# Kernel optimization log

Measured on AMD Instinct MI355X. Metric: run time of the kernel, lower is better.

## Reference

```python
import jax, jax.numpy as jnp
import numpy as np

LMAX = 5
RESOLUTION = 12
ASPECT_RATIO = 2
BATCH = 256
NB = 2 * RESOLUTION                       # res_beta = 24
NA = round(2 * ASPECT_RATIO * RESOLUTION)  # res_alpha = res_gamma = 48
DIM = sum((2 * l + 1) ** 2 for l in range(LMAX + 1))  # 286

# normalize2mom constant for tanh: (E_{z~N(0,1)}[tanh(z)^2])^{-1/2}
_x = np.linspace(-12.0, 12.0, 1_000_001)
_pdf = np.exp(-0.5 * _x * _x) / np.sqrt(2.0 * np.pi)
ACT_CST = float(np.trapz(np.tanh(_x) ** 2 * _pdf, _x) ** -0.5)  # ~1.5927


def _su2_generators(j):
    m = np.arange(-j, j)
    raising = np.diag(-np.sqrt(j * (j + 1) - m * (m + 1)), k=-1).astype(complex)
    m = np.arange(-j + 1, j + 1)
    lowering = np.diag(np.sqrt(j * (j + 1) - m * (m - 1)), k=1).astype(complex)
    m = np.arange(-j, j + 1)
    return np.stack([0.5 * (raising + lowering), np.diag(1j * m), -0.5j * (raising - lowering)])


def _q_real_to_complex(l):
    q = np.zeros((2 * l + 1, 2 * l + 1), dtype=complex)
    for m in range(-l, 0):
        q[l + m, l + abs(m)] = 1 / np.sqrt(2)
        q[l + m, l - abs(m)] = -1j / np.sqrt(2)
    q[l, l] = 1
    for m in range(1, l + 1):
        q[l + m, l + abs(m)] = (-1) ** m / np.sqrt(2)
        q[l + m, l - abs(m)] = 1j * (-1) ** m / np.sqrt(2)
    return (-1j) ** l * q


def _so3_generators(l):
    X = _su2_generators(l)
    Q = _q_real_to_complex(l)
    return np.real(np.conj(Q.T)[None] @ X @ Q[None])  # real [3, 2l+1, 2l+1]


def _expm_angles(A, t):
    """exp(t_n * A) for real antisymmetric A via eigendecomposition. -> [n, d, d] real"""
    vals, vecs = np.linalg.eig(A.astype(complex))
    inv = np.linalg.inv(vecs)
    phases = np.exp(t[:, None] * vals[None, :])  # [n, d]
    return np.real(np.einsum('ij,nj,jk->nik', vecs, phases, inv))


def _build_D_and_qw():
    # Euler angle grids (e3nn SO3Grid convention)
    b = (np.arange(NB) + 0.5) / NB * np.pi          # beta   [nb]
    a = np.arange(NA) / NA * 2.0 * np.pi            # alpha=gamma [na]
    blocks = []
    for l in range(LMAX + 1):
        X = _so3_generators(l)
        Ra = _expm_angles(X[1], a)   # exp(alpha * X1)  [na,d,d]
        Rb = _expm_angles(X[0], b)   # exp(beta  * X0)  [nb,d,d]
        # D^l(a,b,c) = Ra[a] @ Rb[b] @ Ra[c]
        Dl = np.einsum('xij,yjk,zkl->xyzil', Ra, Rb, Ra)
        blocks.append(np.sqrt(2 * l + 1) * Dl.reshape(NA, NB, NA, -1))
    D = np.concatenate(blocks, axis=-1).astype(np.float32)  # [na, nb, na, dim]
    # lie_learn / Kostelec-Rockmore quadrature weights for beta
    bb = NB // 2
    k = np.arange(bb)
    j = np.arange(2 * bb)
    w = (2.0 / bb) * np.sin(np.pi * (2 * j + 1) / (4.0 * bb)) * np.sum(
        (1.0 / (2 * k + 1))[None, :]
        * np.sin((2 * j[:, None] + 1) * (2 * k[None, :] + 1) * np.pi / (4.0 * bb)),
        axis=1,
    )
    w = w / (2.0 * (2 * bb) ** 2)
    qw = (w * NB ** 2 / NA ** 2).astype(np.float32)  # [nb]
    return jnp.asarray(D), jnp.asarray(qw)


def setup_inputs() -> dict:
    key = jax.random.key(0)
    features = jax.random.normal(key, (BATCH, DIM), dtype=jnp.float32)
    D, qw = _build_D_and_qw()
    return {"features": features, "D": D, "qw": qw}


def reference(features, D, qw):
    dim = D.shape[-1]
    s = jnp.sqrt(jnp.asarray(dim, features.dtype))
    # to_grid: [B, dim] x [na, nb, na, dim] -> [B, na, nb, na]
    g = jnp.einsum('bi,xyzi->bxyz', features, D) / s
    # normalized pointwise nonlinearity on SO(3) samples
    g = ACT_CST * jnp.tanh(g)
    # from_grid: quadrature-weighted projection back onto flat Wigner basis
    return jnp.einsum('bxyz,y,xyzi->bi', g, qw, D) * s
```

## Files before the change

### kernel.cpp

```cpp
#include <hip/hip_runtime.h>
#include <hip/hip_bf16.h>

#define DIM    286
#define DIMP   288
#define NZTOT  55296
#define NBATCH 256
#define NB_    24
#define NA_    48
#define ZC     32
#define NTILES 1728
#define NCHUNK 192
#define TILES_PER_WG 9
#define S_CONST 16.911534525287763f
#define INV_S   0.05913123959890826f
#define ACT_CST 1.5927f

typedef short bf16x8 __attribute__((ext_vector_type(8)));
typedef float f32x4  __attribute__((ext_vector_type(4)));

#define WS_FBF  0u
#define WS_DBF  147456u
#define WS_DT   (WS_DBF + 31850496u)
#define WS_PART (WS_DT + 31850496u)

typedef const __attribute__((address_space(1))) char GA;
typedef __attribute__((address_space(3))) char LA;
__device__ __forceinline__ void gload_lds16(const void* g, void* l) {
    __builtin_amdgcn_global_load_lds((GA*)g, (LA*)l, 16, 0, 0);
}

__global__ void k_prep(const float* __restrict__ F, const float* __restrict__ D,
                       const float* __restrict__ qw,
                       __hip_bfloat16* __restrict__ Fbf,
                       __hip_bfloat16* __restrict__ Dbf, __hip_bfloat16* __restrict__ Dt2) {
    __shared__ float T[32][305];
    __shared__ float qs[24];
    int t = threadIdx.x;
    int bid = blockIdx.x;
    if (bid >= NTILES) {
        int o = (bid - NTILES) * 256 + t;
        int row = o / DIMP, col = o % DIMP;
        float v = (col < DIM) ? F[row * DIM + col] * INV_S : 0.f;
        Fbf[o] = __float2bfloat16(v);
        return;
    }
    int z0 = bid * 32;
    if (t < 24) qs[t] = qw[t] * S_CONST;
    const float4* Df = (const float4*)(D + (size_t)z0 * DIM);
    for (int k = 0; k < 9; ++k) {
        int idx = t + k * 256;
        if (idx < 2288) {
            float4 v = Df[idx];
            int e = idx * 4;
            int z = e / DIM, i = e % DIM;
            __hip_bfloat162 lo, hi;
            lo.x = __float2bfloat16(v.x); lo.y = __float2bfloat16(v.y);
            hi.x = __float2bfloat16(v.z); hi.y = __float2bfloat16(v.w);
            T[z][i] = v.x; T[z][i + 1] = v.y;
            *(__hip_bfloat162*)(Dbf + (size_t)(z0 + z) * DIMP + i) = lo;
            if (i == 284) {
                T[z + 1][0] = v.z; T[z + 1][1] = v.w;
                *(__hip_bfloat162*)(Dbf + (size_t)(z0 + z + 1) * DIMP) = hi;
            } else {
                T[z][i + 2] = v.z; T[z][i + 3] = v.w;
                *(__hip_bfloat162*)(Dbf + (size_t)(z0 + z) * DIMP + i + 2) = hi;
            }
        }
    }
    if (t < 32) {
        __hip_bfloat162 zz; zz.x = __float2bfloat16(0.f); zz.y = zz.x;
        *(__hip_bfloat162*)(Dbf + (size_t)(z0 + t) * DIMP + DIM) = zz;
    }
    __syncthreads();
    for (int s = 0; s < 5; ++s) {
        int idx = t + s * 256;
        if (idx < 1152) {
            int i = idx >> 2, zc = idx & 3;
            __hip_bfloat16 o8[8];
            #pragma unroll
            for (int j = 0; j < 8; ++j) {
                int zl = zc * 8 + j;
                int y = ((z0 + zl) / NA_) % NB_;
                o8[j] = __float2bfloat16(T[zl][i] * qs[y]);
            }
            *(bf16x8*)(Dt2 + ((size_t)bid * DIMP + i) * ZC + zc * 8) = *(const bf16x8*)o8;
        }
    }
}

__launch_bounds__(256, 4)
__global__ void k_main(const __hip_bfloat16* __restrict__ Fbf,
                       const __hip_bfloat16* __restrict__ Dbf,
                       const __hip_bfloat16* __restrict__ Dt2,
                       __hip_bfloat16* __restrict__ part) {
    __shared__ __align__(16) __hip_bfloat16 Ds[32][288];
    __shared__ __align__(16) __hip_bfloat16 Dts[288][32];
    __shared__ __align__(16) __hip_bfloat16 Gs[4][16][32];

    int t = threadIdx.x;
    int wave = t >> 6, lane = t & 63, ln = lane & 15, q = lane >> 4;

    bf16x8 fa[9];
    int row = blockIdx.y * 64 + wave * 16 + ln;
    const __hip_bfloat16* fp = Fbf + (size_t)row * DIMP + q * 8;
    #pragma unroll
    for (int ks = 0; ks < 9; ++ks) fa[ks] = *(const bf16x8*)(fp + ks * 32);

    f32x4 acc[18];
    #pragma unroll
    for (int n = 0; n < 18; ++n) acc[n] = (f32x4){0.f, 0.f, 0.f, 0.f};

    #pragma unroll 1
    for (int k = 0; k < TILES_PER_WG; ++k) {
        int tz = blockIdx.x + k * NCHUNK;
        {
            const char* src; char* dst;
            if (wave < 2) {
                src = (const char*)(Dbf + (size_t)tz * ZC * DIMP) + wave * 9216 + lane * 16;
                dst = ((char*)&Ds[0][0]) + wave * 9216;
            } else {
                src = (const char*)(Dt2 + (size_t)tz * DIMP * ZC) + (wave - 2) * 9216 + lane * 16;
                dst = ((char*)&Dts[0][0]) + (wave - 2) * 9216;
            }
            #pragma unroll
            for (int j = 0; j < 9; ++j)
                gload_lds16(src + j * 1024, dst + j * 1024);
        }
        asm volatile("s_waitcnt vmcnt(0)" ::: "memory");
        __syncthreads();
        f32x4 g0 = (f32x4){0.f,0.f,0.f,0.f}, g1 = (f32x4){0.f,0.f,0.f,0.f};
        #pragma unroll
        for (int ks = 0; ks < 9; ++ks) {
            bf16x8 b0 = *(const bf16x8*)(&Ds[ln][ks * 32 + q * 8]);
            bf16x8 b1 = *(const bf16x8*)(&Ds[16 + ln][ks * 32 + q * 8]);
            g0 = __builtin_amdgcn_mfma_f32_16x16x32_bf16(fa[ks], b0, g0, 0, 0, 0);
            g1 = __builtin_amdgcn_mfma_f32_16x16x32_bf16(fa[ks], b1, g1, 0, 0, 0);
        }
        #pragma unroll
        for (int nf = 0; nf < 2; ++nf) {
            #pragma unroll
            for (int r = 0; r < 4; ++r) {
                float x = (nf == 0) ? g0[r] : g1[r];
                float a = fabsf(x);
                float e = __expf(-2.f * a);
                float th = (1.f - e) / (1.f + e);
                float v = copysignf(ACT_CST * th, x);
                Gs[wave][q * 4 + r][nf * 16 + ln] = __float2bfloat16(v);
            }
        }
        bf16x8 a2 = *(const bf16x8*)(&Gs[wave][ln][q * 8]);
        #pragma unroll
        for (int nf = 0; nf < 18; ++nf) {
            bf16x8 b2 = *(const bf16x8*)(&Dts[nf * 16 + ln][q * 8]);
            acc[nf] = __builtin_amdgcn_mfma_f32_16x16x32_bf16(a2, b2, acc[nf], 0, 0, 0);
        }
        __syncthreads();
    }
    __hip_bfloat16* pb = part + ((size_t)blockIdx.x * NBATCH + blockIdx.y * 64 + wave * 16) * DIMP;
    #pragma unroll
    for (int nf = 0; nf < 18; ++nf) {
        #pragma unroll
        for (int r = 0; r < 4; ++r) {
            pb[(size_t)(q * 4 + r) * DIMP + nf * 16 + ln] = __float2bfloat16(acc[nf][r]);
        }
    }
}

__global__ void k_reduce(const __hip_bfloat16* __restrict__ part, float* __restrict__ out) {
    __shared__ float red[3][16][8];
    int t = threadIdx.x, wave = t >> 6, lane = t & 63;
    int j = lane & 15;
    int zg = wave * 4 + (lane >> 4);
    int o8 = blockIdx.x * 16 + j;
    int b = o8 / 36, c8 = o8 % 36;
    const __hip_bfloat16* p = part + (size_t)b * DIMP + c8 * 8;
    float s[8];
    #pragma unroll
    for (int kk = 0; kk < 8; ++kk) s[kk] = 0.f;
    #pragma unroll 4
    for (int ii = 0; ii < 12; ++ii) {
        bf16x8 v = *(const bf16x8*)(p + (size_t)(zg * 12 + ii) * NBATCH * DIMP);
        #pragma unroll
        for (int kk = 0; kk < 8; ++kk) {
            __hip_bfloat16 h; *(short*)&h = v[kk];
            s[kk] += __bfloat162float(h);
        }
    }
    #pragma unroll
    for (int kk = 0; kk < 8; ++kk) {
        s[kk] += __shfl_down(s[kk], 16);
        s[kk] += __shfl_down(s[kk], 32);
    }
    if (wave > 0 && lane < 16) {
        #pragma unroll
        for (int kk = 0; kk < 8; ++kk) red[wave - 1][lane][kk] = s[kk];
    }
    __syncthreads();
    if (wave == 0 && lane < 16) {
        #pragma unroll
        for (int w = 0; w < 3; ++w)
            #pragma unroll
            for (int kk = 0; kk < 8; ++kk) s[kk] += red[w][lane][kk];
        int i0 = c8 * 8;
        #pragma unroll
        for (int kk = 0; kk < 8; ++kk)
            if (i0 + kk < DIM) out[b * DIM + i0 + kk] = s[kk];
    }
}

extern "C" void kernel_launch(void* const* d_in, const int* in_sizes, int n_in,
                              void* d_out, int out_size, void* d_ws, size_t ws_size,
                              hipStream_t stream) {
    const float* F  = (const float*)d_in[0];
    const float* D  = (const float*)d_in[1];
    const float* qw = (const float*)d_in[2];
    char* ws = (char*)d_ws;
    __hip_bfloat16* Fbf = (__hip_bfloat16*)(ws + WS_FBF);
    __hip_bfloat16* Dbf = (__hip_bfloat16*)(ws + WS_DBF);
    __hip_bfloat16* Dt2 = (__hip_bfloat16*)(ws + WS_DT);
    __hip_bfloat16* part = (__hip_bfloat16*)(ws + WS_PART);

    k_prep<<<NTILES + 288, 256, 0, stream>>>(F, D, qw, Fbf, Dbf, Dt2);
    k_main<<<dim3(NCHUNK, 4), 256, 0, stream>>>(Fbf, Dbf, Dt2, part);
    k_reduce<<<576, 256, 0, stream>>>(part, (float*)d_out);
}
```

Before: 159.3 us.

## Process 32 batch rows per wave to halve D tile reloads

Each wave now handles two 16-row batch fragments instead of one, so each workgroup covers 128 batch rows and the grid's y dimension drops from 4 to 2. Each D/Dt tile loaded into LDS is reused across twice as many MFMAs, which halves global/L2 traffic for the large D arrays. The cost is doubled accumulator registers (36 f32x4 plus 18 A fragments), lower occupancy (launch bounds 2), and half as many workgroups, which reduces latency hiding.

```diff
diff --git a/kernel.cpp b/kernel.cpp
--- a/kernel.cpp
+++ b/kernel.cpp
@@ -88,27 +88,32 @@
     }
 }
 
-__launch_bounds__(256, 4)
+__launch_bounds__(256, 2)
 __global__ void k_main(const __hip_bfloat16* __restrict__ Fbf,
                        const __hip_bfloat16* __restrict__ Dbf,
                        const __hip_bfloat16* __restrict__ Dt2,
                        __hip_bfloat16* __restrict__ part) {
     __shared__ __align__(16) __hip_bfloat16 Ds[32][288];
     __shared__ __align__(16) __hip_bfloat16 Dts[288][32];
-    __shared__ __align__(16) __hip_bfloat16 Gs[4][16][32];
+    __shared__ __align__(16) __hip_bfloat16 Gs[4][32][32];
 
     int t = threadIdx.x;
     int wave = t >> 6, lane = t & 63, ln = lane & 15, q = lane >> 4;
 
-    bf16x8 fa[9];
-    int row = blockIdx.y * 64 + wave * 16 + ln;
-    const __hip_bfloat16* fp = Fbf + (size_t)row * DIMP + q * 8;
-    #pragma unroll
-    for (int ks = 0; ks < 9; ++ks) fa[ks] = *(const bf16x8*)(fp + ks * 32);
-
-    f32x4 acc[18];
-    #pragma unroll
-    for (int n = 0; n < 18; ++n) acc[n] = (f32x4){0.f, 0.f, 0.f, 0.f};
+    bf16x8 fa[2][9];
+    int rowbase = blockIdx.y * 128 + wave * 32;
+    #pragma unroll
+    for (int h = 0; h < 2; ++h) {
+        const __hip_bfloat16* fp = Fbf + (size_t)(rowbase + h * 16 + ln) * DIMP + q * 8;
+        #pragma unroll
+        for (int ks = 0; ks < 9; ++ks) fa[h][ks] = *(const bf16x8*)(fp + ks * 32);
+    }
+
+    f32x4 acc[2][18];
+    #pragma unroll
+    for (int h = 0; h < 2; ++h)
+        #pragma unroll
+        for (int n = 0; n < 18; ++n) acc[h][n] = (f32x4){0.f, 0.f, 0.f, 0.f};
 
     #pragma unroll 1
     for (int k = 0; k < TILES_PER_WG; ++k) {
@@ -128,40 +133,52 @@
         }
         asm volatile("s_waitcnt vmcnt(0)" ::: "memory");
         __syncthreads();
-        f32x4 g0 = (f32x4){0.f,0.f,0.f,0.f}, g1 = (f32x4){0.f,0.f,0.f,0.f};
+        f32x4 g00 = (f32x4){0.f,0.f,0.f,0.f}, g01 = (f32x4){0.f,0.f,0.f,0.f};
+        f32x4 g10 = (f32x4){0.f,0.f,0.f,0.f}, g11 = (f32x4){0.f,0.f,0.f,0.f};
         #pragma unroll
         for (int ks = 0; ks < 9; ++ks) {
             bf16x8 b0 = *(const bf16x8*)(&Ds[ln][ks * 32 + q * 8]);
             bf16x8 b1 = *(const bf16x8*)(&Ds[16 + ln][ks * 32 + q * 8]);
-            g0 = __builtin_amdgcn_mfma_f32_16x16x32_bf16(fa[ks], b0, g0, 0, 0, 0);
-            g1 = __builtin_amdgcn_mfma_f32_16x16x32_bf16(fa[ks], b1, g1, 0, 0, 0);
-        }
-        #pragma unroll
-        for (int nf = 0; nf < 2; ++nf) {
-            #pragma unroll
-            for (int r = 0; r < 4; ++r) {
-                float x = (nf == 0) ? g0[r] : g1[r];
-                float a = fabsf(x);
-                float e = __expf(-2.f * a);
-                float th = (1.f - e) / (1.f + e);
-                float v = copysignf(ACT_CST * th, x);
-                Gs[wave][q * 4 + r][nf * 16 + ln] = __float2bfloat16(v);
-            }
-        }
-        bf16x8 a2 = *(const bf16x8*)(&Gs[wave][ln][q * 8]);
+            g00 = __builtin_amdgcn_mfma_f32_16x16x32_bf16(fa[0][ks], b0, g00, 0, 0, 0);
+            g01 = __builtin_amdgcn_mfma_f32_16x16x32_bf16(fa[0][ks], b1, g01, 0, 0, 0);
+            g10 = __builtin_amdgcn_mfma_f32_16x16x32_bf16(fa[1][ks], b0, g10, 0, 0, 0);
+            g11 = __builtin_amdgcn_mfma_f32_16x16x32_bf16(fa[1][ks], b1, g11, 0, 0, 0);
+        }
+        #pragma unroll
+        for (int h = 0; h < 2; ++h) {
+            #pragma unroll
+            for (int zh = 0; zh < 2; ++zh) {
+                f32x4 g = (h == 0) ? (zh == 0 ? g00 : g01) : (zh == 0 ? g10 : g11);
+                #pragma unroll
+                for (int r = 0; r < 4; ++r) {
+                    float x = g[r];
+                    float a = fabsf(x);
+                    float e = __expf(-2.f * a);
+                    float th = (1.f - e) / (1.f + e);
+                    float v = copysignf(ACT_CST * th, x);
+                    Gs[wave][h * 16 + q * 4 + r][zh * 16 + ln] = __float2bfloat16(v);
+                }
+            }
+        }
+        bf16x8 a20 = *(const bf16x8*)(&Gs[wave][ln][q * 8]);
+        bf16x8 a21 = *(const bf16x8*)(&Gs[wave][16 + ln][q * 8]);
         #pragma unroll
         for (int nf = 0; nf < 18; ++nf) {
             bf16x8 b2 = *(const bf16x8*)(&Dts[nf * 16 + ln][q * 8]);
-            acc[nf] = __builtin_amdgcn_mfma_f32_16x16x32_bf16(a2, b2, acc[nf], 0, 0, 0);
+            acc[0][nf] = __builtin_amdgcn_mfma_f32_16x16x32_bf16(a20, b2, acc[0][nf], 0, 0, 0);
+            acc[1][nf] = __builtin_amdgcn_mfma_f32_16x16x32_bf16(a21, b2, acc[1][nf], 0, 0, 0);
         }
         __syncthreads();
     }
-    __hip_bfloat16* pb = part + ((size_t)blockIdx.x * NBATCH + blockIdx.y * 64 + wave * 16) * DIMP;
-    #pragma unroll
-    for (int nf = 0; nf < 18; ++nf) {
-        #pragma unroll
-        for (int r = 0; r < 4; ++r) {
-            pb[(size_t)(q * 4 + r) * DIMP + nf * 16 + ln] = __float2bfloat16(acc[nf][r]);
+    #pragma unroll
+    for (int h = 0; h < 2; ++h) {
+        __hip_bfloat16* pb = part + ((size_t)blockIdx.x * NBATCH + rowbase + h * 16) * DIMP;
+        #pragma unroll
+        for (int nf = 0; nf < 18; ++nf) {
+            #pragma unroll
+            for (int r = 0; r < 4; ++r) {
+                pb[(size_t)(q * 4 + r) * DIMP + nf * 16 + ln] = __float2bfloat16(acc[h][nf][r]);
+            }
         }
     }
 }
@@ -221,6 +238,6 @@
     __hip_bfloat16* part = (__hip_bfloat16*)(ws + WS_PART);
 
     k_prep<<<NTILES + 288, 256, 0, stream>>>(F, D, qw, Fbf, Dbf, Dt2);
-    k_main<<<dim3(NCHUNK, 4), 256, 0, stream>>>(Fbf, Dbf, Dt2, part);
+    k_main<<<dim3(NCHUNK, 2), 256, 0, stream>>>(Fbf, Dbf, Dt2, part);
     k_reduce<<<576, 256, 0, stream>>>(part, (float*)d_out);
 }
```

After: 149.1 us. 1.07x faster.
